# Kernel optimization log

Measured on AMD Instinct MI355X. Metric: run time of the kernel, lower is better.

## Reference

```python
import jax, jax.numpy as jnp
import numpy as np

E, H, O = 64, 128, 16  # enc_hidden_dim, dec_hidden_dim, dec_output_dim (proj_size)
B, N, FUT = 64, 1000, 12


def _lstm_proj_cell(x, h, c, W_ih, W_hh, b_ih, b_hh, W_hr):
    # PyTorch gate order: input, forget, cell(g), output
    gates = x @ W_ih.T + h @ W_hh.T + (b_ih + b_hh)
    i, f, g, o = jnp.split(gates, 4, axis=-1)
    c_new = jax.nn.sigmoid(f) * c + jax.nn.sigmoid(i) * jnp.tanh(g)
    h_full = jax.nn.sigmoid(o) * jnp.tanh(c_new)
    h_new = h_full @ W_hr.T  # proj_size projection
    return h_new, c_new


def setup_inputs() -> dict:
    key = jax.random.key(0)
    ks = jax.random.split(key, 20)
    sc = 0.1
    inp = {
        "enc_outputs": jax.random.normal(ks[0], (B, 1, N, E), jnp.float32),
        "mean": jax.random.normal(ks[1], (B, FUT, N, O), jnp.float32),
        "s": jax.random.normal(ks[2], (1, O), jnp.float32),
        "h_0": jax.random.normal(ks[3], (2, O), jnp.float32),
        "c_0": jax.random.normal(ks[4], (2, H), jnp.float32),
        "W_ih_l0": sc * jax.random.normal(ks[5], (4 * H, E + O), jnp.float32),
        "W_hh_l0": sc * jax.random.normal(ks[6], (4 * H, O), jnp.float32),
        "b_ih_l0": sc * jax.random.normal(ks[7], (4 * H,), jnp.float32),
        "b_hh_l0": sc * jax.random.normal(ks[8], (4 * H,), jnp.float32),
        "W_hr_l0": sc * jax.random.normal(ks[9], (O, H), jnp.float32),
        "W_ih_l1": sc * jax.random.normal(ks[10], (4 * H, O), jnp.float32),
        "W_hh_l1": sc * jax.random.normal(ks[11], (4 * H, O), jnp.float32),
        "b_ih_l1": sc * jax.random.normal(ks[12], (4 * H,), jnp.float32),
        "b_hh_l1": sc * jax.random.normal(ks[13], (4 * H,), jnp.float32),
        "W_hr_l1": sc * jax.random.normal(ks[14], (O, H), jnp.float32),
        "future": FUT,
    }
    # forget-gate bias = 1.0 as in reset_bias()
    for nme in ("b_ih_l0", "b_hh_l0", "b_ih_l1", "b_hh_l1"):
        inp[nme] = inp[nme].at[H:2 * H].set(1.0)
    return inp


def _forward(enc_outputs, mean, s, h_0, c_0,
             W_ih_l0, W_hh_l0, b_ih_l0, b_hh_l0, W_hr_l0,
             W_ih_l1, W_hh_l1, b_ih_l1, b_hh_l1, W_hr_l1, future):
    b, _, n_nodes, _ = enc_outputs.shape
    enc = enc_outputs[:, 0]            # [B, N, E]
    node_mean = jnp.mean(mean, axis=1)  # [B, N, O]
    # state is carried across nodes AND timesteps: one chain of N*future steps
    node_idx = jnp.arange(n_nodes * future) // future

    last0 = jnp.broadcast_to(s[0], (b, s.shape[1]))
    h1_0 = jnp.broadcast_to(h_0[0], (b, h_0.shape[1]))
    h2_0 = jnp.broadcast_to(h_0[1], (b, h_0.shape[1]))
    c1_0 = jnp.broadcast_to(c_0[0], (b, c_0.shape[1]))
    c2_0 = jnp.broadcast_to(c_0[1], (b, c_0.shape[1]))

    def step(carry, n):
        last, h1, c1, h2, c2 = carry
        enc_t = jnp.take(enc, n, axis=1)        # [B, E]
        nm_t = jnp.take(node_mean, n, axis=1)   # [B, O]
        loop = last + nm_t                      # TFRate forced to 0.0 in source
        x = jnp.concatenate([enc_t, loop], axis=-1)
        h1, c1 = _lstm_proj_cell(x, h1, c1, W_ih_l0, W_hh_l0, b_ih_l0, b_hh_l0, W_hr_l0)
        h2, c2 = _lstm_proj_cell(h1, h2, c2, W_ih_l1, W_hh_l1, b_ih_l1, b_hh_l1, W_hr_l1)
        return (h2, h1, c1, h2, c2), h2 + nm_t

    _, outs = jax.lax.scan(step, (last0, h1_0, c1_0, h2_0, c2_0), node_idx)
    # outs: [N*future, B, O] -> [B, future, N, O]
    outs = outs.reshape(n_nodes, future, b, -1).transpose(2, 1, 0, 3)
    return outs


def reference(enc_outputs, mean, s, h_0, c_0,
              W_ih_l0, W_hh_l0, b_ih_l0, b_hh_l0, W_hr_l0,
              W_ih_l1, W_hh_l1, b_ih_l1, b_hh_l1, W_hr_l1, future):
    return _forward(enc_outputs, mean, s, h_0, c_0,
                    W_ih_l0, W_hh_l0, b_ih_l0, b_hh_l0, W_hr_l0,
                    W_ih_l1, W_hh_l1, b_ih_l1, b_hh_l1, W_hr_l1, future)
```

## Files before the change

### kernel.cpp

```cpp
#include <hip/hip_runtime.h>

#define BB 64
#define NN 1000
#define FF 12
#define EE 64
#define HH 128
#define OO 16

__device__ __forceinline__ float rcp_(float x){ return __builtin_amdgcn_rcpf(x); }
__device__ __forceinline__ float tanh_(float x){ return 1.0f - 2.0f*rcp_(__expf(2.0f*x) + 1.0f); }

template<int CTRL>
__device__ __forceinline__ float qswz_(float x){
    int r = __builtin_amdgcn_update_dpp(0, __float_as_int(x), CTRL, 0xF, 0xF, true);
    return __int_as_float(r);
}
__device__ __forceinline__ float bperm_(int byteIdx, float v){
    return __int_as_float(__builtin_amdgcn_ds_bpermute(byteIdx, __float_as_int(v)));
}
__device__ __forceinline__ void barrier_lds_(){
    asm volatile("s_waitcnt lgkmcnt(0)" ::: "memory");
    __builtin_amdgcn_s_barrier();
    asm volatile("" ::: "memory");
}

__global__ __launch_bounds__(512, 2)
void decoder_kernel(const float* __restrict__ enc,
                    const float* __restrict__ mean,
                    const float* __restrict__ sv,
                    const float* __restrict__ h0,
                    const float* __restrict__ c0,
                    const float* __restrict__ Wih0,
                    const float* __restrict__ Whh0,
                    const float* __restrict__ bih0,
                    const float* __restrict__ bhh0,
                    const float* __restrict__ Whr0,
                    const float* __restrict__ Wih1,
                    const float* __restrict__ Whh1,
                    const float* __restrict__ bih1,
                    const float* __restrict__ bhh1,
                    const float* __restrict__ Whr1,
                    float* __restrict__ out)
{
    const int t   = threadIdx.x;
    const int b   = blockIdx.x;
    const int l   = t & 63;
    const int w   = t >> 6;
    const int k   = t >> 2;
    const int tau = t & 3;
    const int g   = tau*HH + k;
    const int pj  = l >> 2;
    const int pc  = l & 3;

    __shared__ __align__(16) float s_h1a[2][OO];
    __shared__ __align__(16) float s_h2a[2][OO];
    __shared__ __align__(16) float s_nm[2][OO];
    __shared__ __align__(16) float s_enc[EE];

    float wl0[16], wh0[16], wi1[16], wh1[16], wq0[4], wq1[4];
    {
        const float4* pL = (const float4*)(Wih0 + (size_t)g*(EE+OO) + EE);
        const float4* pH = (const float4*)(Whh0 + (size_t)g*OO);
        const float4* pI = (const float4*)(Wih1 + (size_t)g*OO);
        const float4* pG = (const float4*)(Whh1 + (size_t)g*OO);
        #pragma unroll
        for (int i=0;i<4;i++){
            float4 v;
            v=pL[i]; wl0[4*i]=v.x; wl0[4*i+1]=v.y; wl0[4*i+2]=v.z; wl0[4*i+3]=v.w;
            v=pH[i]; wh0[4*i]=v.x; wh0[4*i+1]=v.y; wh0[4*i+2]=v.z; wh0[4*i+3]=v.w;
            v=pI[i]; wi1[4*i]=v.x; wi1[4*i+1]=v.y; wi1[4*i+2]=v.z; wi1[4*i+3]=v.w;
            v=pG[i]; wh1[4*i]=v.x; wh1[4*i+1]=v.y; wh1[4*i+2]=v.z; wh1[4*i+3]=v.w;
        }
        float4 q0 = *(const float4*)(Whr0 + (size_t)pj*HH + w*16 + pc*4);
        float4 q1 = *(const float4*)(Whr1 + (size_t)pj*HH + w*16 + pc*4);
        wq0[0]=q0.x; wq0[1]=q0.y; wq0[2]=q0.z; wq0[3]=q0.w;
        wq1[0]=q1.x; wq1[1]=q1.y; wq1[2]=q1.z; wq1[3]=q1.w;
    }
    const float bias0r = bih0[g] + bhh0[g];
    const float bias1r = bih1[g] + bhh1[g];
    float corr1 = 0.f;
    #pragma unroll
    for (int i=0;i<4;i++){
        float4 hv  = *(const float4*)(h0 + OO + 4*i);
        float4 svv = *(const float4*)(sv + 4*i);
        corr1 += (hv.x-svv.x)*wh1[4*i]   + (hv.y-svv.y)*wh1[4*i+1]
               + (hv.z-svv.z)*wh1[4*i+2] + (hv.w-svv.w)*wh1[4*i+3];
    }
    const float am = (tau==2) ? 2.0f : 1.0f;

    float c1v = c0[k];
    float c2v = c0[HH+k];

    const float* encB  = enc  + (size_t)b * NN * EE;
    const float* meanB = mean + (size_t)b * FF * NN * OO;
    float*       outB  = out  + (size_t)b * FF * NN * OO;

    if (t < OO){
        s_h1a[0][t] = h0[t];
        s_h1a[1][t] = 0.f;
        s_h2a[0][t] = sv[t];
        s_h2a[1][t] = 0.f;
        ((float4*)s_enc)[t] = ((const float4*)encB)[t];
    } else if (t < 2*OO){
        const int j = t - OO;
        float a = 0.f;
        #pragma unroll
        for (int ff=0; ff<FF; ++ff) a += meanB[((size_t)ff*NN)*OO + j];
        s_nm[0][j] = a * (1.0f/12.0f);
    }
    __syncthreads();

    float4 ef = make_float4(0.f,0.f,0.f,0.f);
    float nmr[12];
    #pragma unroll
    for (int i=0;i<12;i++) nmr[i]=0.f;
    float pre0 = 0.f;

    int step = 0;
    #pragma unroll 1
    for (int n = 0; n < NN; ++n){
        #pragma unroll 1
        for (int f = 0; f < FF; ++f, ++step){
            const int rp = step & 1;

            float h1v[16], h2v[16];
            {
                const float4* pa = (const float4*)s_h1a[rp];
                const float4* pb = (const float4*)s_h2a[rp];
                #pragma unroll
                for (int i=0;i<4;i++){
                    float4 a = pa[i]; h1v[4*i]=a.x; h1v[4*i+1]=a.y; h1v[4*i+2]=a.z; h1v[4*i+3]=a.w;
                    float4 c = pb[i]; h2v[4*i]=c.x; h2v[4*i+1]=c.y; h2v[4*i+2]=c.z; h2v[4*i+3]=c.w;
                }
            }
            if (step > 0 && t < OO){
                const int fp = (f==0) ? (FF-1) : (f-1);
                const int np = (f==0) ? (n-1)  : n;
                const int sl = (f==0) ? ((n&1)^1) : (n&1);
                outB[((size_t)fp*NN + np)*OO + t] = s_h2a[rp][t] + s_nm[sl][t];
            }
            if (t < OO) s_h2a[rp^1][t] = 0.f;

            if (f == 0){
                float s = bias0r;
                const float4* wp = (const float4*)(Wih0 + (size_t)g*(EE+OO));
                const float4* ep = (const float4*)s_enc;
                #pragma unroll
                for (int e=0;e<16;e++){
                    float4 wv = wp[e], evv = ep[e];
                    s += evv.x*wv.x + evv.y*wv.y + evv.z*wv.z + evv.w*wv.w;
                }
                const float4* nm4 = (const float4*)s_nm[n&1];
                #pragma unroll
                for (int i=0;i<4;i++){
                    float4 m = nm4[i];
                    s += m.x*wl0[4*i] + m.y*wl0[4*i+1] + m.z*wl0[4*i+2] + m.w*wl0[4*i+3];
                }
                pre0 = s;
            }

            float aL=0.f, aH=0.f;
            #pragma unroll
            for (int j=0;j<16;j++){ aL += h2v[j]*wl0[j]; aH += h1v[j]*wh0[j]; }
            float x0  = pre0 + aL + aH;
            float act = 1.f - am * rcp_(__expf(am*x0) + 1.f);

            float r2 = qswz_<0x4E>(act);
            float P  = act * r2;
            float s2 = (tau==1) ? act*c1v : P;
            float cn = s2 + qswz_<0xB1>(s2);
            c1v = cn;
            float tc = tanh_(cn);
            float hf = act * qswz_<0x4E>(tc);

            {
                const int bb = pc*64 + 12;
                float v0 = bperm_(bb,    hf);
                float v1 = bperm_(bb+16, hf);
                float v2 = bperm_(bb+32, hf);
                float v3 = bperm_(bb+48, hf);
                float pr = v0*wq0[0] + v1*wq0[1] + v2*wq0[2] + v3*wq0[3];
                pr += qswz_<0xB1>(pr);
                pr += qswz_<0x4E>(pr);
                if (pc == 0) atomicAdd(&s_h1a[rp^1][pj], pr);
            }
            barrier_lds_();

            float h1n[16];
            {
                const float4* na = (const float4*)s_h1a[rp^1];
                #pragma unroll
                for (int i=0;i<4;i++){
                    float4 a = na[i]; h1n[4*i]=a.x; h1n[4*i+1]=a.y; h1n[4*i+2]=a.z; h1n[4*i+3]=a.w;
                }
            }
            if (t < OO) s_h1a[rp][t] = 0.f;

            if (f == 8 && n+1 < NN){
                if (t < OO){
                    ef = ((const float4*)(encB + (size_t)(n+1)*EE))[t];
                } else if (t < 2*OO){
                    const int j = t - OO;
                    #pragma unroll
                    for (int ff=0; ff<FF; ++ff) nmr[ff] = meanB[((size_t)ff*NN + (n+1))*OO + j];
                }
            }
            if (f == 10 && n+1 < NN){
                if (t < OO){
                    ((float4*)s_enc)[t] = ef;
                } else if (t < 2*OO){
                    float a = 0.f;
                    #pragma unroll
                    for (int ff=0; ff<FF; ++ff) a += nmr[ff];
                    s_nm[(n+1)&1][t-OO] = a * (1.0f/12.0f);
                }
            }

            float aI=0.f, aH2=0.f;
            #pragma unroll
            for (int j=0;j<16;j++){ aI += h1n[j]*wi1[j]; aH2 += h2v[j]*wh1[j]; }
            float x1 = bias1r + aI + aH2;
            if (step == 0) x1 += corr1;
            float act1 = 1.f - am * rcp_(__expf(am*x1) + 1.f);

            float r2b = qswz_<0x4E>(act1);
            float Pb  = act1 * r2b;
            float s2b = (tau==1) ? act1*c2v : Pb;
            float cnb = s2b + qswz_<0xB1>(s2b);
            c2v = cnb;
            float tcb = tanh_(cnb);
            float hf2 = act1 * qswz_<0x4E>(tcb);

            {
                const int bb = pc*64 + 12;
                float v0 = bperm_(bb,    hf2);
                float v1 = bperm_(bb+16, hf2);
                float v2 = bperm_(bb+32, hf2);
                float v3 = bperm_(bb+48, hf2);
                float pr = v0*wq1[0] + v1*wq1[1] + v2*wq1[2] + v3*wq1[3];
                pr += qswz_<0xB1>(pr);
                pr += qswz_<0x4E>(pr);
                if (pc == 0) atomicAdd(&s_h2a[rp^1][pj], pr);
            }
            barrier_lds_();
        }
    }

    if (t < OO)
        outB[((size_t)(FF-1)*NN + (NN-1))*OO + t] = s_h2a[0][t] + s_nm[(NN-1)&1][t];
}

extern "C" void kernel_launch(void* const* d_in, const int* in_sizes, int n_in,
                              void* d_out, int out_size, void* d_ws, size_t ws_size,
                              hipStream_t stream) {
    const float* enc  = (const float*)d_in[0];
    const float* mean = (const float*)d_in[1];
    const float* sv   = (const float*)d_in[2];
    const float* h0   = (const float*)d_in[3];
    const float* c0   = (const float*)d_in[4];
    const float* Wih0 = (const float*)d_in[5];
    const float* Whh0 = (const float*)d_in[6];
    const float* bih0 = (const float*)d_in[7];
    const float* bhh0 = (const float*)d_in[8];
    const float* Whr0 = (const float*)d_in[9];
    const float* Wih1 = (const float*)d_in[10];
    const float* Whh1 = (const float*)d_in[11];
    const float* bih1 = (const float*)d_in[12];
    const float* bhh1 = (const float*)d_in[13];
    const float* Whr1 = (const float*)d_in[14];
    float* out = (float*)d_out;

    decoder_kernel<<<dim3(BB), dim3(512), 0, stream>>>(
        enc, mean, sv, h0, c0,
        Wih0, Whh0, bih0, bhh0, Whr0,
        Wih1, Whh1, bih1, bhh1, Whr1,
        out);
}
```

Baseline: 16.17 ms.

## Replace bpermute projection with DPP/permlane reductions and hoist off-critical-path dot products

```diff
diff --git a/kernel.cpp b/kernel.cpp
--- a/kernel.cpp
+++ b/kernel.cpp
@@ -15,8 +15,18 @@
     int r = __builtin_amdgcn_update_dpp(0, __float_as_int(x), CTRL, 0xF, 0xF, true);
     return __int_as_float(r);
 }
-__device__ __forceinline__ float bperm_(int byteIdx, float v){
-    return __int_as_float(__builtin_amdgcn_ds_bpermute(byteIdx, __float_as_int(v)));
+template<int CTRL>
+__device__ __forceinline__ float dppza_(float v){
+    int s = __builtin_amdgcn_update_dpp(0, __float_as_int(v), CTRL, 0xF, 0xF, true);
+    return v + __int_as_float(s);
+}
+__device__ __forceinline__ float plx32_(float v){
+    float a, b;
+    asm volatile("v_mov_b32 %0, %2\n\t"
+                 "v_mov_b32 %1, %2\n\t"
+                 "v_permlane32_swap_b32 %0, %1"
+                 : "=&v"(a), "=&v"(b) : "v"(v));
+    return a + b;
 }
 __device__ __forceinline__ void barrier_lds_(){
     asm volatile("s_waitcnt lgkmcnt(0)" ::: "memory");
@@ -45,19 +55,16 @@
     const int t   = threadIdx.x;
     const int b   = blockIdx.x;
     const int l   = t & 63;
-    const int w   = t >> 6;
     const int k   = t >> 2;
     const int tau = t & 3;
     const int g   = tau*HH + k;
-    const int pj  = l >> 2;
-    const int pc  = l & 3;
-
-    __shared__ __align__(16) float s_h1a[2][OO];
-    __shared__ __align__(16) float s_h2a[2][OO];
+
+    __shared__ __align__(16) float s_h1a[2][2][16];
+    __shared__ __align__(16) float s_h2a[2][2][16];
     __shared__ __align__(16) float s_nm[2][OO];
     __shared__ __align__(16) float s_enc[EE];
 
-    float wl0[16], wh0[16], wi1[16], wh1[16], wq0[4], wq1[4];
+    float wl0[16], wh0[16], wi1[16], wh1[16], wr0[4], wr1[4];
     {
         const float4* pL = (const float4*)(Wih0 + (size_t)g*(EE+OO) + EE);
         const float4* pH = (const float4*)(Whh0 + (size_t)g*OO);
@@ -71,10 +78,11 @@
             v=pI[i]; wi1[4*i]=v.x; wi1[4*i+1]=v.y; wi1[4*i+2]=v.z; wi1[4*i+3]=v.w;
             v=pG[i]; wh1[4*i]=v.x; wh1[4*i+1]=v.y; wh1[4*i+2]=v.z; wh1[4*i+3]=v.w;
         }
-        float4 q0 = *(const float4*)(Whr0 + (size_t)pj*HH + w*16 + pc*4);
-        float4 q1 = *(const float4*)(Whr1 + (size_t)pj*HH + w*16 + pc*4);
-        wq0[0]=q0.x; wq0[1]=q0.y; wq0[2]=q0.z; wq0[3]=q0.w;
-        wq1[0]=q1.x; wq1[1]=q1.y; wq1[2]=q1.z; wq1[3]=q1.w;
+        #pragma unroll
+        for (int u=0;u<4;u++){
+            wr0[u] = Whr0[(size_t)(4*tau+u)*HH + k];
+            wr1[u] = Whr1[(size_t)(4*tau+u)*HH + k];
+        }
     }
     const float bias0r = bih0[g] + bhh0[g];
     const float bias1r = bih1[g] + bhh1[g];
@@ -95,11 +103,13 @@
     const float* meanB = mean + (size_t)b * FF * NN * OO;
     float*       outB  = out  + (size_t)b * FF * NN * OO;
 
+    if (t < 32){
+        ((float*)s_h1a[0])[t] = 0.f;
+        ((float*)s_h1a[1])[t] = 0.f;
+        ((float*)s_h2a[1])[t] = 0.f;
+        ((float*)s_h2a[0])[t] = (t < OO) ? sv[t] : 0.f;
+    }
     if (t < OO){
-        s_h1a[0][t] = h0[t];
-        s_h1a[1][t] = 0.f;
-        s_h2a[0][t] = sv[t];
-        s_h2a[1][t] = 0.f;
         ((float4*)s_enc)[t] = ((const float4*)encB)[t];
     } else if (t < 2*OO){
         const int j = t - OO;
@@ -110,11 +120,40 @@
     }
     __syncthreads();
 
+    float aH_pre;
+    {
+        float y0=0,y1=0,y2=0,y3=0;
+        #pragma unroll
+        for (int i=0;i<4;i++){
+            y0 += h0[i]   *wh0[i];    y1 += h0[4+i] *wh0[4+i];
+            y2 += h0[8+i] *wh0[8+i];  y3 += h0[12+i]*wh0[12+i];
+        }
+        aH_pre = (y0+y1)+(y2+y3);
+    }
+    float pre0;
+    {
+        float s = bias0r;
+        const float4* wp = (const float4*)(Wih0 + (size_t)g*(EE+OO));
+        const float4* ep = (const float4*)s_enc;
+        #pragma unroll
+        for (int e=0;e<16;e++){
+            float4 wv = wp[e], ev = ep[e];
+            s += ev.x*wv.x + ev.y*wv.y + ev.z*wv.z + ev.w*wv.w;
+        }
+        const float4* nm4 = (const float4*)s_nm[0];
+        #pragma unroll
+        for (int i=0;i<4;i++){
+            float4 m = nm4[i];
+            s += m.x*wl0[4*i] + m.y*wl0[4*i+1] + m.z*wl0[4*i+2] + m.w*wl0[4*i+3];
+        }
+        pre0 = s;
+    }
+
     float4 ef = make_float4(0.f,0.f,0.f,0.f);
     float nmr[12];
     #pragma unroll
     for (int i=0;i<12;i++) nmr[i]=0.f;
-    float pre0 = 0.f;
+    float aH2_pre = 0.f;
 
     int step = 0;
     #pragma unroll 1
@@ -123,47 +162,36 @@
         for (int f = 0; f < FF; ++f, ++step){
             const int rp = step & 1;
 
-            float h1v[16], h2v[16];
-            {
-                const float4* pa = (const float4*)s_h1a[rp];
-                const float4* pb = (const float4*)s_h2a[rp];
-                #pragma unroll
-                for (int i=0;i<4;i++){
-                    float4 a = pa[i]; h1v[4*i]=a.x; h1v[4*i+1]=a.y; h1v[4*i+2]=a.z; h1v[4*i+3]=a.w;
-                    float4 c = pb[i]; h2v[4*i]=c.x; h2v[4*i+1]=c.y; h2v[4*i+2]=c.z; h2v[4*i+3]=c.w;
+            float h2v[16];
+            {
+                const float4* ga = (const float4*)&s_h2a[rp][0][0];
+                const float4* gb = (const float4*)&s_h2a[rp][1][0];
+                #pragma unroll
+                for (int i=0;i<4;i++){
+                    float4 a = ga[i], c = gb[i];
+                    h2v[4*i]=a.x+c.x; h2v[4*i+1]=a.y+c.y; h2v[4*i+2]=a.z+c.z; h2v[4*i+3]=a.w+c.w;
                 }
             }
             if (step > 0 && t < OO){
                 const int fp = (f==0) ? (FF-1) : (f-1);
                 const int np = (f==0) ? (n-1)  : n;
                 const int sl = (f==0) ? ((n&1)^1) : (n&1);
-                outB[((size_t)fp*NN + np)*OO + t] = s_h2a[rp][t] + s_nm[sl][t];
-            }
-            if (t < OO) s_h2a[rp^1][t] = 0.f;
-
-            if (f == 0){
-                float s = bias0r;
-                const float4* wp = (const float4*)(Wih0 + (size_t)g*(EE+OO));
-                const float4* ep = (const float4*)s_enc;
-                #pragma unroll
-                for (int e=0;e<16;e++){
-                    float4 wv = wp[e], evv = ep[e];
-                    s += evv.x*wv.x + evv.y*wv.y + evv.z*wv.z + evv.w*wv.w;
-                }
-                const float4* nm4 = (const float4*)s_nm[n&1];
-                #pragma unroll
-                for (int i=0;i<4;i++){
-                    float4 m = nm4[i];
-                    s += m.x*wl0[4*i] + m.y*wl0[4*i+1] + m.z*wl0[4*i+2] + m.w*wl0[4*i+3];
-                }
-                pre0 = s;
-            }
-
-            float aL=0.f, aH=0.f;
-            #pragma unroll
-            for (int j=0;j<16;j++){ aL += h2v[j]*wl0[j]; aH += h1v[j]*wh0[j]; }
-            float x0  = pre0 + aL + aH;
-            float act = 1.f - am * rcp_(__expf(am*x0) + 1.f);
+                outB[((size_t)fp*NN + np)*OO + t] = s_h2a[rp][0][t] + s_h2a[rp][1][t] + s_nm[sl][t];
+            }
+            if (t < 32) ((float*)s_h2a[rp^1])[t] = 0.f;
+
+            float aL;
+            {
+                float x0=0,x1=0,x2=0,x3=0;
+                #pragma unroll
+                for (int i=0;i<4;i++){
+                    x0 += h2v[i]   *wl0[i];    x1 += h2v[4+i] *wl0[4+i];
+                    x2 += h2v[8+i] *wl0[8+i];  x3 += h2v[12+i]*wl0[12+i];
+                }
+                aL = (x0+x1)+(x2+x3);
+            }
+            float xg  = pre0 + aL + aH_pre;
+            float act = 1.f - am * rcp_(__expf(am*xg) + 1.f);
 
             float r2 = qswz_<0x4E>(act);
             float P  = act * r2;
@@ -174,27 +202,40 @@
             float hf = act * qswz_<0x4E>(tc);
 
             {
-                const int bb = pc*64 + 12;
-                float v0 = bperm_(bb,    hf);
-                float v1 = bperm_(bb+16, hf);
-                float v2 = bperm_(bb+32, hf);
-                float v3 = bperm_(bb+48, hf);
-                float pr = v0*wq0[0] + v1*wq0[1] + v2*wq0[2] + v3*wq0[3];
-                pr += qswz_<0xB1>(pr);
-                pr += qswz_<0x4E>(pr);
-                if (pc == 0) atomicAdd(&s_h1a[rp^1][pj], pr);
+                float hb = qswz_<0xFF>(hf);
+                float p0 = hb*wr0[0], p1 = hb*wr0[1], p2 = hb*wr0[2], p3 = hb*wr0[3];
+                p0 = dppza_<0x114>(p0); p1 = dppza_<0x114>(p1); p2 = dppza_<0x114>(p2); p3 = dppza_<0x114>(p3);
+                p0 = dppza_<0x118>(p0); p1 = dppza_<0x118>(p1); p2 = dppza_<0x118>(p2); p3 = dppza_<0x118>(p3);
+                p0 = plx32_(p0); p1 = plx32_(p1); p2 = plx32_(p2); p3 = plx32_(p3);
+                if (l < 32 && (l & 12) == 12){
+                    float* dst = &s_h1a[rp^1][l>>4][4*tau];
+                    atomicAdd(dst+0, p0); atomicAdd(dst+1, p1);
+                    atomicAdd(dst+2, p2); atomicAdd(dst+3, p3);
+                }
+            }
+
+            {
+                float y0=0,y1=0,y2=0,y3=0;
+                #pragma unroll
+                for (int i=0;i<4;i++){
+                    y0 += h2v[i]   *wh1[i];    y1 += h2v[4+i] *wh1[4+i];
+                    y2 += h2v[8+i] *wh1[8+i];  y3 += h2v[12+i]*wh1[12+i];
+                }
+                aH2_pre = (y0+y1)+(y2+y3);
             }
             barrier_lds_();
 
             float h1n[16];
             {
-                const float4* na = (const float4*)s_h1a[rp^1];
-                #pragma unroll
-                for (int i=0;i<4;i++){
-                    float4 a = na[i]; h1n[4*i]=a.x; h1n[4*i+1]=a.y; h1n[4*i+2]=a.z; h1n[4*i+3]=a.w;
-                }
-            }
-            if (t < OO) s_h1a[rp][t] = 0.f;
+                const float4* ga = (const float4*)&s_h1a[rp^1][0][0];
+                const float4* gb = (const float4*)&s_h1a[rp^1][1][0];
+                #pragma unroll
+                for (int i=0;i<4;i++){
+                    float4 a = ga[i], c = gb[i];
+                    h1n[4*i]=a.x+c.x; h1n[4*i+1]=a.y+c.y; h1n[4*i+2]=a.z+c.z; h1n[4*i+3]=a.w+c.w;
+                }
+            }
+            if (t < 32) ((float*)s_h1a[rp])[t] = 0.f;
 
             if (f == 8 && n+1 < NN){
                 if (t < OO){
@@ -216,12 +257,19 @@
                 }
             }
 
-            float aI=0.f, aH2=0.f;
-            #pragma unroll
-            for (int j=0;j<16;j++){ aI += h1n[j]*wi1[j]; aH2 += h2v[j]*wh1[j]; }
-            float x1 = bias1r + aI + aH2;
-            if (step == 0) x1 += corr1;
-            float act1 = 1.f - am * rcp_(__expf(am*x1) + 1.f);
+            float aI;
+            {
+                float x0=0,x1=0,x2=0,x3=0;
+                #pragma unroll
+                for (int i=0;i<4;i++){
+                    x0 += h1n[i]   *wi1[i];    x1 += h1n[4+i] *wi1[4+i];
+                    x2 += h1n[8+i] *wi1[8+i];  x3 += h1n[12+i]*wi1[12+i];
+                }
+                aI = (x0+x1)+(x2+x3);
+            }
+            float xg1 = bias1r + aI + aH2_pre;
+            if (step == 0) xg1 += corr1;
+            float act1 = 1.f - am * rcp_(__expf(am*xg1) + 1.f);
 
             float r2b = qswz_<0x4E>(act1);
             float Pb  = act1 * r2b;
@@ -232,22 +280,52 @@
             float hf2 = act1 * qswz_<0x4E>(tcb);
 
             {
-                const int bb = pc*64 + 12;
-                float v0 = bperm_(bb,    hf2);
-                float v1 = bperm_(bb+16, hf2);
-                float v2 = bperm_(bb+32, hf2);
-                float v3 = bperm_(bb+48, hf2);
-                float pr = v0*wq1[0] + v1*wq1[1] + v2*wq1[2] + v3*wq1[3];
-                pr += qswz_<0xB1>(pr);
-                pr += qswz_<0x4E>(pr);
-                if (pc == 0) atomicAdd(&s_h2a[rp^1][pj], pr);
+                float hb = qswz_<0xFF>(hf2);
+                float p0 = hb*wr1[0], p1 = hb*wr1[1], p2 = hb*wr1[2], p3 = hb*wr1[3];
+                p0 = dppza_<0x114>(p0); p1 = dppza_<0x114>(p1); p2 = dppza_<0x114>(p2); p3 = dppza_<0x114>(p3);
+                p0 = dppza_<0x118>(p0); p1 = dppza_<0x118>(p1); p2 = dppza_<0x118>(p2); p3 = dppza_<0x118>(p3);
+                p0 = plx32_(p0); p1 = plx32_(p1); p2 = plx32_(p2); p3 = plx32_(p3);
+                if (l < 32 && (l & 12) == 12){
+                    float* dst = &s_h2a[rp^1][l>>4][4*tau];
+                    atomicAdd(dst+0, p0); atomicAdd(dst+1, p1);
+                    atomicAdd(dst+2, p2); atomicAdd(dst+3, p3);
+                }
+            }
+
+            {
+                float y0=0,y1=0,y2=0,y3=0;
+                #pragma unroll
+                for (int i=0;i<4;i++){
+                    y0 += h1n[i]   *wh0[i];    y1 += h1n[4+i] *wh0[4+i];
+                    y2 += h1n[8+i] *wh0[8+i];  y3 += h1n[12+i]*wh0[12+i];
+                }
+                aH_pre = (y0+y1)+(y2+y3);
+            }
+
+            if (f == 11 && n+1 < NN){
+                float s = bias0r;
+                const float4* wp = (const float4*)(Wih0 + (size_t)g*(EE+OO));
+                const float4* ep = (const float4*)s_enc;
+                #pragma unroll
+                for (int e=0;e<16;e++){
+                    float4 wv = wp[e], ev = ep[e];
+                    s += ev.x*wv.x + ev.y*wv.y + ev.z*wv.z + ev.w*wv.w;
+                }
+                const float4* nm4 = (const float4*)s_nm[(n+1)&1];
+                #pragma unroll
+                for (int i=0;i<4;i++){
+                    float4 m = nm4[i];
+                    s += m.x*wl0[4*i] + m.y*wl0[4*i+1] + m.z*wl0[4*i+2] + m.w*wl0[4*i+3];
+                }
+                pre0 = s;
             }
             barrier_lds_();
         }
     }
 
     if (t < OO)
-        outB[((size_t)(FF-1)*NN + (NN-1))*OO + t] = s_h2a[0][t] + s_nm[(NN-1)&1][t];
+        outB[((size_t)(FF-1)*NN + (NN-1))*OO + t] =
+            s_h2a[0][0][t] + s_h2a[0][1][t] + s_nm[(NN-1)&1][t];
 }
 
 extern "C" void kernel_launch(void* const* d_in, const int* in_sizes, int n_in,
```

Result: slower. 20.59 ms (+27.3%).
